# Optimization experiments

Hardware: AMD Instinct MI355X
Metric: run time of the kernel (lower is better)

## Reference

```python
import jax, jax.numpy as jnp
import numpy as np

N_FEAT = 8
N_HIDDEN = 3
N_NEURONS = 16
N_ENERGY = 4


def setup_inputs() -> dict:
    key = jax.random.key(0)
    ks = jax.random.split(key, 2 * N_HIDDEN + 2)
    inp = {"features": jax.random.normal(ks[0], (16, 512, 512, N_FEAT), dtype=jnp.float32)}
    d_in = N_FEAT
    for i in range(N_HIDDEN):
        bound = 1.0 / np.sqrt(d_in)
        inp[f"W{i}"] = jax.random.uniform(ks[2 * i + 1], (d_in, N_NEURONS), minval=-bound, maxval=bound, dtype=jnp.float32)
        inp[f"b{i}"] = jax.random.uniform(ks[2 * i + 2], (N_NEURONS,), minval=-bound, maxval=bound, dtype=jnp.float32)
        inp[f"g{i}"] = jnp.ones((N_NEURONS,), jnp.float32)   # LayerNorm gamma
        inp[f"be{i}"] = jnp.zeros((N_NEURONS,), jnp.float32)  # LayerNorm beta
        d_in = N_NEURONS
    bound = 1.0 / np.sqrt(d_in)
    inp["Wo"] = jax.random.uniform(ks[-1], (d_in, N_ENERGY), minval=-bound, maxval=bound, dtype=jnp.float32)
    inp["bo"] = jnp.zeros((N_ENERGY,), jnp.float32)
    return inp


def _layernorm(x, g, b, eps=1e-5):
    mu = jnp.mean(x, axis=-1, keepdims=True)
    var = jnp.mean(jnp.square(x - mu), axis=-1, keepdims=True)
    return (x - mu) * jax.lax.rsqrt(var + eps) * g + b


def reference(features, W0, b0, g0, be0, W1, b1, g1, be1, W2, b2, g2, be2, Wo, bo):
    B, Nx, Ny, F = features.shape
    x = features.reshape(B * Nx * Ny, F)
    for W, b, g, be in ((W0, b0, g0, be0), (W1, b1, g1, be1), (W2, b2, g2, be2)):
        x = jax.nn.gelu(_layernorm(x @ W + b, g, be), approximate=False)
    z = x @ Wo + bo
    f_a = 1.0 + jnp.tanh(z)
    return f_a.reshape(B, Nx, Ny, -1)
```

## Files before the change

kernel.cpp:

```cpp
#include <hip/hip_runtime.h>
#include <type_traits>

#define BLOCK 256
#define WAVES_PER_BLOCK 4
#define NBLOCKS 4096
#define TILES_PER_WAVE 8
#define QUADS (TILES_PER_WAVE/4)

typedef __fp16 f16;
typedef f16 f16x2 __attribute__((ext_vector_type(2)));
typedef f16 f16x8 __attribute__((ext_vector_type(8)));
typedef float f32x2 __attribute__((ext_vector_type(2)));
typedef float f32x16 __attribute__((ext_vector_type(16)));
typedef unsigned u32x2 __attribute__((ext_vector_type(2)));

__device__ __forceinline__ float ex2(float x){ return __builtin_amdgcn_exp2f(x); }
__device__ __forceinline__ float rcp_(float x){ return __builtin_amdgcn_rcpf(x); }
__device__ __forceinline__ float rsq_(float x){ return __builtin_amdgcn_rsqf(x); }

__device__ __forceinline__ f32x2 mk2(float a, float b){
    f32x2 r; r.x = a; r.y = b; return r;
}

__device__ __forceinline__ unsigned pk2(float a, float b){
    f16x2 h = __builtin_amdgcn_cvt_pkrtz(a, b);
    union { f16x2 h; unsigned u; } cv; cv.h = h; return cv.u;
}

__device__ __forceinline__ u32x2 plswap(unsigned a, unsigned b){
    return __builtin_amdgcn_permlane32_swap(a, b, false, false);
}
__device__ __forceinline__ float xhalf_sum(float x){
    union { float f; unsigned u; } cvt; cvt.f = x;
    u32x2 r = plswap(cvt.u, cvt.u);
    union { unsigned u; float f; } lo, hi; lo.u = r.x; hi.u = r.y;
    return lo.f + hi.f;
}

__device__ __forceinline__ float gelu_ref(float v){
    float av = fabsf(v);
    float e  = ex2(v*v * -0.7213475204444817f);
    float t  = rcp_(fmaf(0.23164190157f, av, 1.0f));
    float p  = fmaf(fmaf(fmaf(fmaf(1.061405429f, t, -1.453152027f), t,
                              1.421413741f), t, -0.284496736f), t, 0.254829592f);
    float pt = p * t;
    float erfabs = fmaf(-pt, e, 1.0f);
    return 0.5f * fmaf(av, erfabs, v);
}

union U8 { f16x8 v; unsigned u[4]; };
union PU { f16x2 v; unsigned u; };

__global__ __launch_bounds__(BLOCK) void nn_kernel(
    const float* __restrict__ feat,
    const float* __restrict__ W0, const float* __restrict__ b0v,
    const float* __restrict__ g0v, const float* __restrict__ be0v,
    const float* __restrict__ W1, const float* __restrict__ b1v,
    const float* __restrict__ g1v, const float* __restrict__ be1v,
    const float* __restrict__ W2, const float* __restrict__ b2v,
    const float* __restrict__ g2v, const float* __restrict__ be2v,
    const float* __restrict__ Wo, const float* __restrict__ bov,
    float* __restrict__ out)
{
    __shared__ __align__(16) f16   tabH[4096];
    __shared__ __align__(16) float cb[3][16];
    __shared__ __align__(16) float cg[3][16];
    __shared__ __align__(16) float cbe[3][16];
    __shared__ __align__(16) float cbo[4];

    const int tid = threadIdx.x;
    if (tid < 16){
        cb[0][tid]  = b0v[tid];  cb[1][tid]  = b1v[tid];  cb[2][tid]  = b2v[tid];
        cg[0][tid]  = g0v[tid];  cg[1][tid]  = g1v[tid];  cg[2][tid]  = g2v[tid];
        cbe[0][tid] = be0v[tid]; cbe[1][tid] = be1v[tid]; cbe[2][tid] = be2v[tid];
    }
    if (tid < 4) cbo[tid] = bov[tid];
    for (int i = tid; i < 4096; i += BLOCK){
        float v = (float)(i - 2048) * (1.0f/512.0f) + (0.5f/512.0f);
        tabH[i] = (f16)gelu_ref(v);
    }
    __syncthreads();

    const int lane = tid & 63;
    const int wv   = tid >> 6;
    const int gg   = lane >> 5;
    const int c    = lane & 31;

    U8 aW0, aW1, aW2, aWo;
    {
        float w[8];
        #pragma unroll
        for (int j=0;j<8;++j){
            if (gg==0) w[j] = (c<16) ? W0[j*16 + c] : 0.f;
            else       w[j] = (j==0 && c<16) ? b0v[c] : 0.f;
        }
        aW0.u[0]=pk2(w[0],w[1]); aW0.u[1]=pk2(w[2],w[3]);
        aW0.u[2]=pk2(w[4],w[5]); aW0.u[3]=pk2(w[6],w[7]);
        #pragma unroll
        for (int j=0;j<8;++j) w[j] = (c<16) ? W1[(gg*8+j)*16 + c] : 0.f;
        aW1.u[0]=pk2(w[0],w[1]); aW1.u[1]=pk2(w[2],w[3]);
        aW1.u[2]=pk2(w[4],w[5]); aW1.u[3]=pk2(w[6],w[7]);
        #pragma unroll
        for (int j=0;j<8;++j) w[j] = (c<16) ? W2[(gg*8+j)*16 + c] : 0.f;
        aW2.u[0]=pk2(w[0],w[1]); aW2.u[1]=pk2(w[2],w[3]);
        aW2.u[2]=pk2(w[4],w[5]); aW2.u[3]=pk2(w[6],w[7]);
        const int eidx = (c < 2) ? c : ((c == 4 || c == 5) ? (c - 2) : -1);
        #pragma unroll
        for (int j=0;j<8;++j) w[j] = (eidx >= 0) ? Wo[(gg*8+j)*4 + eidx] : 0.f;
        aWo.u[0]=pk2(w[0],w[1]); aWo.u[1]=pk2(w[2],w[3]);
        aWo.u[2]=pk2(w[4],w[5]); aWo.u[3]=pk2(w[6],w[7]);
    }

    bool okl = true;
    if (lane < 16){
        #pragma unroll
        for (int l=0;l<3;++l)
            okl = okl && (cg[l][lane]==1.0f) && (cbe[l][lane]==0.0f);
    }
    const bool triv = (__ballot(okl) == 0xFFFFFFFFFFFFFFFFull);

    const int n0 = 4*gg, n1 = 8 + 4*gg;
    const float4 b1q0 = *(const float4*)&cb[1][n0], b1q1 = *(const float4*)&cb[1][n1];
    const float4 b2q0 = *(const float4*)&cb[2][n0], b2q1 = *(const float4*)&cb[2][n1];
    const f32x2 b1p0 = mk2(b1q0.x,b1q0.y), b1p1 = mk2(b1q0.z,b1q0.w);
    const f32x2 b1p2 = mk2(b1q1.x,b1q1.y), b1p3 = mk2(b1q1.z,b1q1.w);
    const f32x2 b2p0 = mk2(b2q0.x,b2q0.y), b2p1 = mk2(b2q0.z,b2q0.w);
    const f32x2 b2p2 = mk2(b2q1.x,b2q1.y), b2p3 = mk2(b2q1.z,b2q1.w);
    const float K = 2.8853900817779268f;
    const f32x2 K2   = mk2(K, K);
    const f32x2 bo22 = mk2(cbo[2*gg]*K, cbo[2*gg+1]*K);

    f32x16 zC;
    #pragma unroll
    for (int i=0;i<16;++i) zC[i]=0.f;

    const long gw = (long)blockIdx.x * WAVES_PER_BLOCK + wv;
    const long rowbase = gw * (TILES_PER_WAVE*32L);
    const char* fb = (const char*)feat + (rowbase + c) * 32L;
    char*       ob = (char*)out        + (rowbase + c) * 16L + gg*8;

    auto body = [&](auto TRIVC){
        constexpr bool TRIV = decltype(TRIVC)::value;

        auto lnact = [&](f32x2 h01, f32x2 h23, f32x2 h45, f32x2 h67, int l) -> U8 {
            f32x2 sp = (h01 + h23) + (h45 + h67);
            float s  = sp.x + sp.y;
            f32x2 q  = h01 * h01;
            q = __builtin_elementwise_fma(h23, h23, q);
            q = __builtin_elementwise_fma(h45, h45, q);
            q = __builtin_elementwise_fma(h67, h67, q);
            float s2 = q.x + q.y;
            s  = xhalf_sum(s);
            s2 = xhalf_sum(s2);
            const float mu  = s * 0.0625f;
            const float var = fmaf(-mu, mu, s2 * 0.0625f);
            const float rs  = rsq_(var + 1e-5f);

            PU p0, p1, p2, p3;
            if constexpr (TRIV){
                const float Ri = rs * 512.f;
                const float Ni = fmaf(-mu, Ri, 2048.f);
                const f32x2 R2 = mk2(Ri, Ri), N2 = mk2(Ni, Ni);
                f32x2 i01 = __builtin_elementwise_fma(h01, R2, N2);
                f32x2 i23 = __builtin_elementwise_fma(h23, R2, N2);
                f32x2 i45 = __builtin_elementwise_fma(h45, R2, N2);
                f32x2 i67 = __builtin_elementwise_fma(h67, R2, N2);
                p0.v.x = tabH[(int)i01.x]; p0.v.y = tabH[(int)i01.y];
                p1.v.x = tabH[(int)i23.x]; p1.v.y = tabH[(int)i23.y];
                p2.v.x = tabH[(int)i45.x]; p2.v.y = tabH[(int)i45.y];
                p3.v.x = tabH[(int)i67.x]; p3.v.y = tabH[(int)i67.y];
            } else {
                const float nm = -mu * rs;
                const float4 gq0 = *(const float4*)&cg[l][n0];
                const float4 gq1 = *(const float4*)&cg[l][n1];
                const float4 eq0 = *(const float4*)&cbe[l][n0];
                const float4 eq1 = *(const float4*)&cbe[l][n1];
                const float hv[8] = {h01.x,h01.y,h23.x,h23.y,h45.x,h45.y,h67.x,h67.y};
                const float ga[8] = {gq0.x,gq0.y,gq0.z,gq0.w, gq1.x,gq1.y,gq1.z,gq1.w};
                const float ba[8] = {eq0.x,eq0.y,eq0.z,eq0.w, eq1.x,eq1.y,eq1.z,eq1.w};
                float xf[8];
                #pragma unroll
                for (int i=0;i<8;++i){
                    float t  = fmaf(hv[i], rs, nm);
                    t = fmaf(t, ga[i], ba[i]);
                    xf[i] = fminf(fmaxf(fmaf(t, 512.f, 2048.f), 0.f), 4095.f);
                }
                p0.v.x = tabH[(int)xf[0]]; p0.v.y = tabH[(int)xf[1]];
                p1.v.x = tabH[(int)xf[2]]; p1.v.y = tabH[(int)xf[3]];
                p2.v.x = tabH[(int)xf[4]]; p2.v.y = tabH[(int)xf[5]];
                p3.v.x = tabH[(int)xf[6]]; p3.v.y = tabH[(int)xf[7]];
            }
            u32x2 e0 = plswap(p0.u, p2.u);
            u32x2 e1 = plswap(p1.u, p3.u);
            U8 F;
            F.u[0] = e0.x; F.u[1] = e1.x; F.u[2] = e0.y; F.u[3] = e1.y;
            return F;
        };

        #pragma unroll 1
        for (int q = 0; q < QUADS; ++q){
            const char* fq = fb + q*4096L;

            float4 t0a = *(const float4*)(fq +    0), t0b = *(const float4*)(fq +   16);
            float4 t1a = *(const float4*)(fq + 1024), t1b = *(const float4*)(fq + 1040);
            float4 t2a = *(const float4*)(fq + 2048), t2b = *(const float4*)(fq + 2064);
            float4 t3a = *(const float4*)(fq + 3072), t3b = *(const float4*)(fq + 3088);

            U8 B0, B1, B2, B3;
            B0.u[0]=pk2(t0a.x,t0a.y); B0.u[1]=pk2(t0a.z,t0a.w);
            B0.u[2]=pk2(t0b.x,t0b.y); B0.u[3]=pk2(t0b.z,t0b.w);
            B1.u[0]=pk2(t1a.x,t1a.y); B1.u[1]=pk2(t1a.z,t1a.w);
            B1.u[2]=pk2(t1b.x,t1b.y); B1.u[3]=pk2(t1b.z,t1b.w);
            B2.u[0]=pk2(t2a.x,t2a.y); B2.u[1]=pk2(t2a.z,t2a.w);
            B2.u[2]=pk2(t2b.x,t2b.y); B2.u[3]=pk2(t2b.z,t2b.w);
            B3.u[0]=pk2(t3a.x,t3a.y); B3.u[1]=pk2(t3a.z,t3a.w);
            B3.u[2]=pk2(t3b.x,t3b.y); B3.u[3]=pk2(t3b.z,t3b.w);
            if (gg){
                B0.u[0]=0x00003C00u; B1.u[0]=0x00003C00u;
                B2.u[0]=0x00003C00u; B3.u[0]=0x00003C00u;
            }

            f32x16 h0 = __builtin_amdgcn_mfma_f32_32x32x16_f16(aW0.v, B0.v, zC, 0,0,0);
            f32x16 h1 = __builtin_amdgcn_mfma_f32_32x32x16_f16(aW0.v, B1.v, zC, 0,0,0);
            f32x16 h2 = __builtin_amdgcn_mfma_f32_32x32x16_f16(aW0.v, B2.v, zC, 0,0,0);
            f32x16 h3 = __builtin_amdgcn_mfma_f32_32x32x16_f16(aW0.v, B3.v, zC, 0,0,0);

            U8 F0 = lnact(mk2(h0[0],h0[1]), mk2(h0[2],h0[3]), mk2(h0[4],h0[5]), mk2(h0[6],h0[7]), 0);
            U8 F1 = lnact(mk2(h1[0],h1[1]), mk2(h1[2],h1[3]), mk2(h1[4],h1[5]), mk2(h1[6],h1[7]), 0);
            U8 F2 = lnact(mk2(h2[0],h2[1]), mk2(h2[2],h2[3]), mk2(h2[4],h2[5]), mk2(h2[6],h2[7]), 0);
            U8 F3 = lnact(mk2(h3[0],h3[1]), mk2(h3[2],h3[3]), mk2(h3[4],h3[5]), mk2(h3[6],h3[7]), 0);

            h0 = __builtin_amdgcn_mfma_f32_32x32x16_f16(aW1.v, F0.v, zC, 0,0,0);
            h1 = __builtin_amdgcn_mfma_f32_32x32x16_f16(aW1.v, F1.v, zC, 0,0,0);
            h2 = __builtin_amdgcn_mfma_f32_32x32x16_f16(aW1.v, F2.v, zC, 0,0,0);
            h3 = __builtin_amdgcn_mfma_f32_32x32x16_f16(aW1.v, F3.v, zC, 0,0,0);
            F0 = lnact(mk2(h0[0],h0[1])+b1p0, mk2(h0[2],h0[3])+b1p1,
                       mk2(h0[4],h0[5])+b1p2, mk2(h0[6],h0[7])+b1p3, 1);
            F1 = lnact(mk2(h1[0],h1[1])+b1p0, mk2(h1[2],h1[3])+b1p1,
                       mk2(h1[4],h1[5])+b1p2, mk2(h1[6],h1[7])+b1p3, 1);
            F2 = lnact(mk2(h2[0],h2[1])+b1p0, mk2(h2[2],h2[3])+b1p1,
                       mk2(h2[4],h2[5])+b1p2, mk2(h2[6],h2[7])+b1p3, 1);
            F3 = lnact(mk2(h3[0],h3[1])+b1p0, mk2(h3[2],h3[3])+b1p1,
                       mk2(h3[4],h3[5])+b1p2, mk2(h3[6],h3[7])+b1p3, 1);

            h0 = __builtin_amdgcn_mfma_f32_32x32x16_f16(aW2.v, F0.v, zC, 0,0,0);
            h1 = __builtin_amdgcn_mfma_f32_32x32x16_f16(aW2.v, F1.v, zC, 0,0,0);
            h2 = __builtin_amdgcn_mfma_f32_32x32x16_f16(aW2.v, F2.v, zC, 0,0,0);
            h3 = __builtin_amdgcn_mfma_f32_32x32x16_f16(aW2.v, F3.v, zC, 0,0,0);
            F0 = lnact(mk2(h0[0],h0[1])+b2p0, mk2(h0[2],h0[3])+b2p1,
                       mk2(h0[4],h0[5])+b2p2, mk2(h0[6],h0[7])+b2p3, 2);
            F1 = lnact(mk2(h1[0],h1[1])+b2p0, mk2(h1[2],h1[3])+b2p1,
                       mk2(h1[4],h1[5])+b2p2, mk2(h1[6],h1[7])+b2p3, 2);
            F2 = lnact(mk2(h2[0],h2[1])+b2p0, mk2(h2[2],h2[3])+b2p1,
                       mk2(h2[4],h2[5])+b2p2, mk2(h2[6],h2[7])+b2p3, 2);
            F3 = lnact(mk2(h3[0],h3[1])+b2p0, mk2(h3[2],h3[3])+b2p1,
                       mk2(h3[4],h3[5])+b2p2, mk2(h3[6],h3[7])+b2p3, 2);

            h0 = __builtin_amdgcn_mfma_f32_32x32x16_f16(aWo.v, F0.v, zC, 0,0,0);
            h1 = __builtin_amdgcn_mfma_f32_32x32x16_f16(aWo.v, F1.v, zC, 0,0,0);
            h2 = __builtin_amdgcn_mfma_f32_32x32x16_f16(aWo.v, F2.v, zC, 0,0,0);
            h3 = __builtin_amdgcn_mfma_f32_32x32x16_f16(aWo.v, F3.v, zC, 0,0,0);

            f32x2 z0 = __builtin_elementwise_fma(mk2(h0[0],h0[1]), K2, bo22);
            f32x2 z1 = __builtin_elementwise_fma(mk2(h1[0],h1[1]), K2, bo22);
            f32x2 z2 = __builtin_elementwise_fma(mk2(h2[0],h2[1]), K2, bo22);
            f32x2 z3 = __builtin_elementwise_fma(mk2(h3[0],h3[1]), K2, bo22);
            float2 r0, r1, r2, r3;
            r0.x = fmaf(-2.0f, rcp_(ex2(z0.x)+1.0f), 2.0f);
            r0.y = fmaf(-2.0f, rcp_(ex2(z0.y)+1.0f), 2.0f);
            r1.x = fmaf(-2.0f, rcp_(ex2(z1.x)+1.0f), 2.0f);
            r1.y = fmaf(-2.0f, rcp_(ex2(z1.y)+1.0f), 2.0f);
            r2.x = fmaf(-2.0f, rcp_(ex2(z2.x)+1.0f), 2.0f);
            r2.y = fmaf(-2.0f, rcp_(ex2(z2.y)+1.0f), 2.0f);
            r3.x = fmaf(-2.0f, rcp_(ex2(z3.x)+1.0f), 2.0f);
            r3.y = fmaf(-2.0f, rcp_(ex2(z3.y)+1.0f), 2.0f);
            *(float2*)(ob + q*2048L       ) = r0;
            *(float2*)(ob + q*2048L +  512) = r1;
            *(float2*)(ob + q*2048L + 1024) = r2;
            *(float2*)(ob + q*2048L + 1536) = r3;
        }
    };

    if (triv) body(std::integral_constant<bool,true>{});
    else      body(std::integral_constant<bool,false>{});
}

extern "C" void kernel_launch(void* const* d_in, const int* in_sizes, int n_in,
                              void* d_out, int out_size, void* d_ws, size_t ws_size,
                              hipStream_t stream) {
    const float* feat = (const float*)d_in[0];
    const float* W0  = (const float*)d_in[1];
    const float* b0  = (const float*)d_in[2];
    const float* g0  = (const float*)d_in[3];
    const float* be0 = (const float*)d_in[4];
    const float* W1  = (const float*)d_in[5];
    const float* b1  = (const float*)d_in[6];
    const float* g1  = (const float*)d_in[7];
    const float* be1 = (const float*)d_in[8];
    const float* W2  = (const float*)d_in[9];
    const float* b2  = (const float*)d_in[10];
    const float* g2  = (const float*)d_in[11];
    const float* be2 = (const float*)d_in[12];
    const float* Wo  = (const float*)d_in[13];
    const float* bo  = (const float*)d_in[14];
    float* out = (float*)d_out;

    hipLaunchKernelGGL(nn_kernel, dim3(NBLOCKS), dim3(BLOCK), 0, stream,
                       feat, W0, b0, g0, be0, W1, b1, g1, be1,
                       W2, b2, g2, be2, Wo, bo, out);
}
```

Measured before the change: 85.73 us.

## Prefetch next quad's first tiles, duplicate GELU table per half-wave, set occupancy bound

The first two feature tiles of the next quad are now loaded early, so global load latency overlaps with the current quad's MFMA and LayerNorm work. The GELU lookup table is duplicated in LDS, one copy per half-wave, to spread table lookups across banks and reduce conflicts. launch_bounds now requests 4 blocks per CU, which caps register use. The prefetch holds extra live registers and doubles the table's LDS footprint, which together with the tighter register cap could cause spills.

```diff
diff --git a/kernel.cpp b/kernel.cpp
--- a/kernel.cpp
+++ b/kernel.cpp
@@ -51,7 +51,7 @@
 union U8 { f16x8 v; unsigned u[4]; };
 union PU { f16x2 v; unsigned u; };
 
-__global__ __launch_bounds__(BLOCK) void nn_kernel(
+__global__ __launch_bounds__(BLOCK, 4) void nn_kernel(
     const float* __restrict__ feat,
     const float* __restrict__ W0, const float* __restrict__ b0v,
     const float* __restrict__ g0v, const float* __restrict__ be0v,
@@ -62,7 +62,7 @@
     const float* __restrict__ Wo, const float* __restrict__ bov,
     float* __restrict__ out)
 {
-    __shared__ __align__(16) f16   tabH[4096];
+    __shared__ __align__(16) f16   tabH[2][4096];
     __shared__ __align__(16) float cb[3][16];
     __shared__ __align__(16) float cg[3][16];
     __shared__ __align__(16) float cbe[3][16];
@@ -77,7 +77,9 @@
     if (tid < 4) cbo[tid] = bov[tid];
     for (int i = tid; i < 4096; i += BLOCK){
         float v = (float)(i - 2048) * (1.0f/512.0f) + (0.5f/512.0f);
-        tabH[i] = (f16)gelu_ref(v);
+        f16 g = (f16)gelu_ref(v);
+        tabH[0][i] = g;
+        tabH[1][i] = g;
     }
     __syncthreads();
 
@@ -85,6 +87,7 @@
     const int wv   = tid >> 6;
     const int gg   = lane >> 5;
     const int c    = lane & 31;
+    const f16* __restrict__ tb = &tabH[gg][0];
 
     U8 aW0, aW1, aW2, aWo;
     {
@@ -165,10 +168,10 @@
                 f32x2 i23 = __builtin_elementwise_fma(h23, R2, N2);
                 f32x2 i45 = __builtin_elementwise_fma(h45, R2, N2);
                 f32x2 i67 = __builtin_elementwise_fma(h67, R2, N2);
-                p0.v.x = tabH[(int)i01.x]; p0.v.y = tabH[(int)i01.y];
-                p1.v.x = tabH[(int)i23.x]; p1.v.y = tabH[(int)i23.y];
-                p2.v.x = tabH[(int)i45.x]; p2.v.y = tabH[(int)i45.y];
-                p3.v.x = tabH[(int)i67.x]; p3.v.y = tabH[(int)i67.y];
+                p0.v.x = tb[(int)i01.x]; p0.v.y = tb[(int)i01.y];
+                p1.v.x = tb[(int)i23.x]; p1.v.y = tb[(int)i23.y];
+                p2.v.x = tb[(int)i45.x]; p2.v.y = tb[(int)i45.y];
+                p3.v.x = tb[(int)i67.x]; p3.v.y = tb[(int)i67.y];
             } else {
                 const float nm = -mu * rs;
                 const float4 gq0 = *(const float4*)&cg[l][n0];
@@ -185,10 +188,10 @@
                     t = fmaf(t, ga[i], ba[i]);
                     xf[i] = fminf(fmaxf(fmaf(t, 512.f, 2048.f), 0.f), 4095.f);
                 }
-                p0.v.x = tabH[(int)xf[0]]; p0.v.y = tabH[(int)xf[1]];
-                p1.v.x = tabH[(int)xf[2]]; p1.v.y = tabH[(int)xf[3]];
-                p2.v.x = tabH[(int)xf[4]]; p2.v.y = tabH[(int)xf[5]];
-                p3.v.x = tabH[(int)xf[6]]; p3.v.y = tabH[(int)xf[7]];
+                p0.v.x = tb[(int)xf[0]]; p0.v.y = tb[(int)xf[1]];
+                p1.v.x = tb[(int)xf[2]]; p1.v.y = tb[(int)xf[3]];
+                p2.v.x = tb[(int)xf[4]]; p2.v.y = tb[(int)xf[5]];
+                p3.v.x = tb[(int)xf[6]]; p3.v.y = tb[(int)xf[7]];
             }
             u32x2 e0 = plswap(p0.u, p2.u);
             u32x2 e1 = plswap(p1.u, p3.u);
@@ -197,20 +200,21 @@
             return F;
         };
 
+        float4 p0a = *(const float4*)(fb +    0), p0b = *(const float4*)(fb +   16);
+        float4 p1a = *(const float4*)(fb + 1024), p1b = *(const float4*)(fb + 1040);
+
         #pragma unroll 1
         for (int q = 0; q < QUADS; ++q){
             const char* fq = fb + q*4096L;
 
-            float4 t0a = *(const float4*)(fq +    0), t0b = *(const float4*)(fq +   16);
-            float4 t1a = *(const float4*)(fq + 1024), t1b = *(const float4*)(fq + 1040);
             float4 t2a = *(const float4*)(fq + 2048), t2b = *(const float4*)(fq + 2064);
             float4 t3a = *(const float4*)(fq + 3072), t3b = *(const float4*)(fq + 3088);
 
             U8 B0, B1, B2, B3;
-            B0.u[0]=pk2(t0a.x,t0a.y); B0.u[1]=pk2(t0a.z,t0a.w);
-            B0.u[2]=pk2(t0b.x,t0b.y); B0.u[3]=pk2(t0b.z,t0b.w);
-            B1.u[0]=pk2(t1a.x,t1a.y); B1.u[1]=pk2(t1a.z,t1a.w);
-            B1.u[2]=pk2(t1b.x,t1b.y); B1.u[3]=pk2(t1b.z,t1b.w);
+            B0.u[0]=pk2(p0a.x,p0a.y); B0.u[1]=pk2(p0a.z,p0a.w);
+            B0.u[2]=pk2(p0b.x,p0b.y); B0.u[3]=pk2(p0b.z,p0b.w);
+            B1.u[0]=pk2(p1a.x,p1a.y); B1.u[1]=pk2(p1a.z,p1a.w);
+            B1.u[2]=pk2(p1b.x,p1b.y); B1.u[3]=pk2(p1b.z,p1b.w);
             B2.u[0]=pk2(t2a.x,t2a.y); B2.u[1]=pk2(t2a.z,t2a.w);
             B2.u[2]=pk2(t2b.x,t2b.y); B2.u[3]=pk2(t2b.z,t2b.w);
             B3.u[0]=pk2(t3a.x,t3a.y); B3.u[1]=pk2(t3a.z,t3a.w);
@@ -218,6 +222,12 @@
             if (gg){
                 B0.u[0]=0x00003C00u; B1.u[0]=0x00003C00u;
                 B2.u[0]=0x00003C00u; B3.u[0]=0x00003C00u;
+            }
+
+            {
+                const char* pn = fb + ((q+1 < QUADS) ? (q+1) : q)*4096L;
+                p0a = *(const float4*)(pn +    0); p0b = *(const float4*)(pn +   16);
+                p1a = *(const float4*)(pn + 1024); p1b = *(const float4*)(pn + 1040);
             }
 
             f32x16 h0 = __builtin_amdgcn_mfma_f32_32x32x16_f16(aW0.v, B0.v, zC, 0,0,0);
```

After: 112.1 us. 1.31x slower.
